# Performance work log

Measured on AMD Instinct MI355X. Metric: run time of the kernel, lower is better.

The kernel has to match this reference:

```python
import jax, jax.numpy as jnp
import numpy as np

ALPHA = (0.02, 0.04, 0.08, 0.16)
CHAMFER_W, SMOOTH_W, CURVATURE_W = 1.0, 1.0, 0.3
NS = (8192, 4096, 2048, 1024)
B = 2


def _sqdist(a, b):
    # a: [B,N,3], b: [B,M,3] -> [B,N,M] squared euclidean distance
    return (jnp.sum(a * a, axis=-1)[:, :, None]
            - 2.0 * jnp.einsum('bnc,bmc->bnm', a, b)
            + jnp.sum(b * b, axis=-1)[:, None, :])


def _knn(d, k):
    # k smallest distances + indices along last axis
    neg, idx = jax.lax.top_k(-d, k)
    return -neg, idx


def _gather(points, idx):
    # points: [B,M,C], idx: [B,N,K] -> [B,N,K,C]
    return jax.vmap(lambda p, i: p[i])(points, idx)


def _scale_loss(pc1, pc2, flow):
    # pc1, pc2, flow: [B,3,N]-like -> permute to points-last layout
    p1 = jnp.transpose(pc1, (0, 2, 1))   # [B,N,3]
    p2 = jnp.transpose(pc2, (0, 2, 1))   # [B,M,3]
    fl = jnp.transpose(flow, (0, 2, 1))  # [B,N,3]
    warp = p1 + fl                        # warped pc1

    # curvature of pc2 (10-NN on pc2 itself)
    _, k22 = _knn(_sqdist(p2, p2), 10)
    cv2 = jnp.sum(_gather(p2, k22) - p2[:, :, None, :], axis=2) / 9.0  # [B,M,3]

    # 10-NN on pc1 (shared for warped curvature and smoothness; 9-NN is prefix)
    _, k11 = _knn(_sqdist(p1, p1), 10)
    cvw = jnp.sum(_gather(warp, k11) - warp[:, :, None, :], axis=2) / 9.0  # [B,N,3]

    k9 = k11[:, :, :9]
    gfl = _gather(fl, k9)  # [B,N,9,3]
    smooth = jnp.sum(jnp.linalg.norm(gfl - fl[:, :, None, :], axis=3), axis=2) / 8.0  # [B,N]

    # chamfer between warped pc1 and pc2
    d12 = _sqdist(warp, p2)               # [B,N,M]
    dist1 = jnp.min(d12, axis=-1)         # [B,N]
    dist2 = jnp.min(d12, axis=1)          # [B,M]

    # inverse-distance interpolation of pc2 curvature onto warped pc1 (5-NN)
    dist, kidx = _knn(d12, 5)             # [B,N,5]
    gcv = _gather(cv2, kidx)              # [B,N,5,3]
    w = 1.0 / (dist + 1e-8)
    w = w / jnp.sum(w, axis=2, keepdims=True)
    inter = jnp.sum(w[..., None] * gcv, axis=2)  # [B,N,3]

    chamfer = jnp.mean(jnp.sum(dist1, axis=1)) + jnp.mean(jnp.sum(dist2, axis=1))
    smoothness = jnp.mean(jnp.sum(smooth, axis=1))
    curv = jnp.mean(jnp.sum(jnp.sum((inter - cvw) ** 2, axis=2), axis=1))
    return chamfer, smoothness, curv


def setup_inputs() -> dict:
    key = jax.random.key(0)
    keys = jax.random.split(key, 12)
    out = {}
    names = ['pc1', 'pc2', 'flow']
    k = 0
    for name in names:
        for i, n in enumerate(NS):
            scale = 1.0 if name != 'flow' else 0.1
            out[f'{name}_{i}'] = scale * jax.random.normal(keys[k], (B, 3, n), dtype=jnp.float32)
            k += 1
    return out


def reference(pc1_0, pc1_1, pc1_2, pc1_3,
              pc2_0, pc2_1, pc2_2, pc2_3,
              flow_0, flow_1, flow_2, flow_3):
    pcs1 = (pc1_0, pc1_1, pc1_2, pc1_3)
    pcs2 = (pc2_0, pc2_1, pc2_2, pc2_3)
    flows = (flow_0, flow_1, flow_2, flow_3)
    ch = sm = cv = jnp.float32(0.0)
    for a, p1, p2, fl in zip(ALPHA, pcs1, pcs2, flows):
        c, s, k = _scale_loss(p1, p2, fl)
        ch = ch + a * c
        sm = sm + a * s
        cv = cv + a * k
    total = CHAMFER_W * ch + CURVATURE_W * cv + SMOOTH_W * sm
    return jnp.reshape(total, (1,))
```

## Files before the change

### kernel.cpp

```cpp
#include <hip/hip_runtime.h>
#include <math.h>


#define BLOCK 512
#define UNIT 1024
#define NTOT 15360
#define MASKC 0xFFFFE000u
#define PB 340

typedef unsigned int uint;

struct Params {
  const float* pc1[4];
  const float* pc2[4];
  const float* fl[4];
  float4* cv2;
  float4* cvw;
  float* keys;
  float* out;
};

__device__ __forceinline__ void decode(int r, int wv, int& s, int& b,
                                       int& i0, int& lo, int& N, int& cpw,
                                       int& off, float& alpha) {
  int rr;
  if (r < 256)      { s = 0; rr = r; }
  else if (r < 320) { s = 1; rr = r - 256; }
  else if (r < 336) { s = 2; rr = r - 320; }
  else              { s = 3; rr = r - 336; }
  N = 8192 >> s;
  cpw = 8 >> s;
  int perb = 128 >> (2 * s);
  b = rr >> (7 - 2 * s);
  int chunk = rr & (perb - 1);
  int qg = (chunk << s) + (wv >> (3 - s));
  i0 = qg << 6;
  lo = (wv & (cpw - 1)) << 10;
  off = 16384 - (16384 >> s);
  alpha = 0.02f * (float)(1 << s);
}

__device__ __forceinline__ float wave_sum(float v) {
  #pragma unroll
  for (int o = 32; o; o >>= 1) v += __shfl_down(v, o, 64);
  return v;
}

template <int K>
__device__ __forceinline__ void key_insert(float (&kd)[K], float kf) {
  #pragma unroll
  for (int m = K - 1; m >= 1; --m)
    kd[m] = __builtin_amdgcn_fmed3f(kf, kd[m - 1], kd[m]);
  kd[0] = fminf(kd[0], kf);
}

template <int K>
__device__ __forceinline__ void merge_pair(float (&a)[K], const float (&b)[K]) {
  #pragma unroll
  for (int m = 0; m < K; ++m) key_insert<K>(a, b[m]);
}

__device__ __forceinline__ float pack_key(float d, float iw) {
  return __uint_as_float((__float_as_uint(d) & MASKC) | __float_as_uint(iw));
}

template <int K, bool WARP, bool PACK>
__device__ void scan_u(const float* px, const float* py, const float* pz,
                       const float* fx, const float* fy, const float* fz,
                       int lo, float ax, float ay, float az,
                       float (&a)[K], float (&b)[K], float4* tile,
                       int lane) {
  int j = lo + lane;
  float x = px[j], y = py[j], z = pz[j];
  if (WARP) { x += fx[j]; y += fy[j]; z += fz[j]; }
  for (int c0 = lo; c0 < lo + UNIT; c0 += 64) {
    tile[lane] = make_float4(x, y, z, __uint_as_float((uint)(c0 + lane)));
    asm volatile("s_waitcnt lgkmcnt(0)" ::: "memory");
    if (c0 + 64 < lo + UNIT) {
      int jn = j + 64;
      x = px[jn]; y = py[jn]; z = pz[jn];
      if (WARP) { x += fx[jn]; y += fy[jn]; z += fz[jn]; }
    }
    #pragma unroll 8
    for (int t = 0; t < 64; t += 2) {
      float4 cA = tile[t];
      float4 cB = tile[t + 1];
      float dxa = ax - cA.x, dya = ay - cA.y, dza = az - cA.z;
      float dA = fmaf(dxa, dxa, fmaf(dya, dya, dza * dza));
      float dxb = ax - cB.x, dyb = ay - cB.y, dzb = az - cB.z;
      float dB = fmaf(dxb, dxb, fmaf(dyb, dyb, dzb * dzb));
      if (PACK) {
        key_insert<K>(a, pack_key(dA, cA.w));
        key_insert<K>(b, pack_key(dB, cB.w));
      } else {
        a[0] = fminf(a[0], dA);
        b[0] = fminf(b[0], dB);
      }
    }
    j += 64;
  }
}

template <int K>
__device__ __forceinline__ bool merge_group(float (&a)[K], float* sm,
                                            int tid, int cpw) {
  const int STR = K | 1;
  int q = tid & 63, wv = tid >> 6;
  #pragma unroll
  for (int m = 0; m < K; ++m) sm[(wv * 64 + q) * STR + m] = a[m];
  __syncthreads();
  if (wv & (cpw - 1)) return false;
  for (int w = wv + 1; w < wv + cpw; ++w)
    #pragma unroll
    for (int m = 0; m < K; ++m)
      key_insert<K>(a, sm[(w * 64 + q) * STR + m]);
  return true;
}

__global__ __launch_bounds__(1) void k_zero(float* out) { out[0] = 0.f; }

__global__ __launch_bounds__(BLOCK, 8) void k_fused(Params P) {
  __shared__ float4 tiles[8][64];
  __shared__ float sm[8 * 64 * 11];
  int tid = threadIdx.x, q = tid & 63, wv = tid >> 6;
  int pass = blockIdx.x / PB, r = blockIdx.x % PB;
  int s, b, i0, lo, N, cpw, off; float alpha;
  decode(r, wv, s, b, i0, lo, N, cpw, off, alpha);
  int i = i0 + q;
  float4* tile = tiles[wv];

  if (pass == 0) {
    const float* p2 = P.pc2[s] + b * 3 * N;
    float ax = p2[i], ay = p2[N + i], az = p2[2 * N + i];
    float a[10], bb[10];
    #pragma unroll
    for (int m = 0; m < 10; ++m) { a[m] = 3.0e38f; bb[m] = 3.0e38f; }
    scan_u<10, false, true>(p2, p2 + N, p2 + 2 * N, nullptr, nullptr,
                            nullptr, lo, ax, ay, az, a, bb, tile, q);
    merge_pair<10>(a, bb);
    if (!merge_group<10>(a, sm, tid, cpw)) return;
    float sx = 0.f, sy = 0.f, sz = 0.f;
    #pragma unroll
    for (int m = 0; m < 10; ++m) {
      int j = (int)(__float_as_uint(a[m]) & 0x1FFFu);
      sx += p2[j]; sy += p2[N + j]; sz += p2[2 * N + j];
    }
    const float inv9 = 1.f / 9.f;
    P.cv2[b * NTOT + off + i] = make_float4((sx - 10.f * ax) * inv9,
                                            (sy - 10.f * ay) * inv9,
                                            (sz - 10.f * az) * inv9, 0.f);
  } else if (pass == 1) {
    const float* p1 = P.pc1[s] + b * 3 * N;
    const float* fl = P.fl[s] + b * 3 * N;
    float ax = p1[i], ay = p1[N + i], az = p1[2 * N + i];
    float a[10], bb[10];
    #pragma unroll
    for (int m = 0; m < 10; ++m) { a[m] = 3.0e38f; bb[m] = 3.0e38f; }
    scan_u<10, false, true>(p1, p1 + N, p1 + 2 * N, nullptr, nullptr,
                            nullptr, lo, ax, ay, az, a, bb, tile, q);
    merge_pair<10>(a, bb);
    if (!merge_group<10>(a, sm, tid, cpw)) return;
    float fix = fl[i], fiy = fl[N + i], fiz = fl[2 * N + i];
    float wix = ax + fix, wiy = ay + fiy, wiz = az + fiz;
    float sx = 0.f, sy = 0.f, sz = 0.f, smooth = 0.f;
    float dmax = -1.f, worst = 0.f;
    #pragma unroll
    for (int m = 0; m < 10; ++m) {
      int j = (int)(__float_as_uint(a[m]) & 0x1FFFu);
      float px = p1[j], py = p1[N + j], pz = p1[2 * N + j];
      float flx = fl[j], fly = fl[N + j], flz = fl[2 * N + j];
      sx += px + flx; sy += py + fly; sz += pz + flz;
      float ddx = px - ax, ddy = py - ay, ddz = pz - az;
      float d = fmaf(ddx, ddx, fmaf(ddy, ddy, ddz * ddz));
      float gx = flx - fix, gy = fly - fiy, gz = flz - fiz;
      float term = sqrtf(fmaf(gx, gx, fmaf(gy, gy, gz * gz)));
      smooth += term;
      if (d > dmax) { dmax = d; worst = term; }
    }
    smooth -= worst;
    const float inv9 = 1.f / 9.f;
    P.cvw[b * NTOT + off + i] = make_float4((sx - 10.f * wix) * inv9,
                                            (sy - 10.f * wiy) * inv9,
                                            (sz - 10.f * wiz) * inv9, 0.f);
    float ssum = wave_sum(smooth * (1.f / 8.f));
    if (q == 0) atomicAdd(P.out, alpha * 0.5f * ssum);
  } else if (pass == 2) {
    const float* p1 = P.pc1[s] + b * 3 * N;
    const float* fl = P.fl[s] + b * 3 * N;
    const float* p2 = P.pc2[s] + b * 3 * N;
    float ax = p2[i], ay = p2[N + i], az = p2[2 * N + i];
    float a[1], bb[1];
    a[0] = 3.0e38f; bb[0] = 3.0e38f;
    scan_u<1, true, false>(p1, p1 + N, p1 + 2 * N, fl, fl + N, fl + 2 * N,
                           lo, ax, ay, az, a, bb, tile, q);
    merge_pair<1>(a, bb);
    if (!merge_group<1>(a, sm, tid, cpw)) return;
    float msum = wave_sum(a[0]);
    if (q == 0) atomicAdd(P.out, alpha * 0.5f * msum);
  } else {
    const float* p1 = P.pc1[s] + b * 3 * N;
    const float* fl = P.fl[s] + b * 3 * N;
    const float* p2 = P.pc2[s] + b * 3 * N;
    float ax = p1[i] + fl[i], ay = p1[N + i] + fl[N + i],
          az = p1[2 * N + i] + fl[2 * N + i];
    float a[5], bb[5];
    #pragma unroll
    for (int m = 0; m < 5; ++m) { a[m] = 3.0e38f; bb[m] = 3.0e38f; }
    scan_u<5, false, true>(p2, p2 + N, p2 + 2 * N, nullptr, nullptr,
                           nullptr, lo, ax, ay, az, a, bb, tile, q);
    merge_pair<5>(a, bb);
    if (!merge_group<5>(a, sm, tid, cpw)) return;
    #pragma unroll
    for (int m = 0; m < 5; ++m)
      P.keys[m * (2 * NTOT) + b * NTOT + off + i] = a[m];
  }
}

__global__ __launch_bounds__(256) void k_epi(Params P) {
  int t = blockIdx.x * 256 + threadIdx.x;
  int b = t >= NTOT;
  int r = t - b * NTOT;
  int s, i;
  if (r < 8192)       { s = 0; i = r; }
  else if (r < 12288) { s = 1; i = r - 8192; }
  else if (r < 14336) { s = 2; i = r - 12288; }
  else                { s = 3; i = r - 14336; }
  int N = 8192 >> s;
  int off = 16384 - (16384 >> s);
  float alpha = 0.02f * (float)(1 << s);
  const float* p1 = P.pc1[s] + b * 3 * N;
  const float* fl = P.fl[s] + b * 3 * N;
  const float* p2 = P.pc2[s] + b * 3 * N;
  float ax = p1[i] + fl[i], ay = p1[N + i] + fl[N + i],
        az = p1[2 * N + i] + fl[2 * N + i];
  float dist1 = 3.0e38f, wsum = 0.f, ix = 0.f, iy = 0.f, iz = 0.f;
  #pragma unroll
  for (int m = 0; m < 5; ++m) {
    uint key = __float_as_uint(P.keys[m * (2 * NTOT) + b * NTOT + off + i]);
    int j = (int)(key & 0x1FFFu);
    float px = p2[j], py = p2[N + j], pz = p2[2 * N + j];
    float ddx = px - ax, ddy = py - ay, ddz = pz - az;
    float d = fmaf(ddx, ddx, fmaf(ddy, ddy, ddz * ddz));
    dist1 = fminf(dist1, d);
    float w = 1.f / (d + 1e-8f);
    wsum += w;
    float4 cv = P.cv2[b * NTOT + off + j];
    ix += w * cv.x; iy += w * cv.y; iz += w * cv.z;
  }
  float inv = 1.f / wsum;
  ix *= inv; iy *= inv; iz *= inv;
  float4 cw = P.cvw[b * NTOT + off + i];
  float ex = ix - cw.x, ey = iy - cw.y, ez = iz - cw.z;
  float curv = fmaf(ex, ex, fmaf(ey, ey, ez * ez));
  float v = alpha * 0.5f * (dist1 + 0.3f * curv);
  v = wave_sum(v);
  if ((threadIdx.x & 63) == 0) atomicAdd(P.out, v);
}

extern "C" void kernel_launch(void* const* d_in, const int* in_sizes, int n_in,
                              void* d_out, int out_size, void* d_ws,
                              size_t ws_size, hipStream_t stream) {
  Params P;
  for (int s = 0; s < 4; ++s) {
    P.pc1[s] = (const float*)d_in[s];
    P.pc2[s] = (const float*)d_in[4 + s];
    P.fl[s]  = (const float*)d_in[8 + s];
  }
  P.cv2 = (float4*)d_ws;
  P.cvw = (float4*)((char*)d_ws + (size_t)2 * NTOT * sizeof(float4));
  P.keys = (float*)((char*)d_ws + (size_t)4 * NTOT * sizeof(float4));
  P.out = (float*)d_out;

  k_zero<<<dim3(1), dim3(1), 0, stream>>>(P.out);
  k_fused<<<dim3(4 * PB), dim3(BLOCK), 0, stream>>>(P);
  k_epi<<<dim3((2 * NTOT) / 256), dim3(256), 0, stream>>>(P);
}
```

Measured before the change: 309.0 us.

## Stream candidate points via scalar loads instead of LDS tiles in kNN scans

The per-wave LDS tile staging of candidate points is replaced by wave-uniform scalar s_load_dwordx8 loads of eight candidates per coordinate into SGPRs, which the distance computation then uses directly. This removes LDS writes and reads and the lgkmcnt waits on the tile, and the packed index is now computed from a uniform counter instead of being stored in the tile. In exchange, every 8-candidate step waits on its scalar loads with no prefetch overlap and goes through the scalar cache, which may stall the inner loop, especially in the warped-chamfer scan that issues six loads per step.

Result: slower. 315.2 us (+2.0%).

```diff
diff --git a/kernel.cpp b/kernel.cpp
--- a/kernel.cpp
+++ b/kernel.cpp
@@ -9,6 +9,7 @@
 #define PB 340
 
 typedef unsigned int uint;
+typedef __attribute__((ext_vector_type(8))) float f8;
 
 struct Params {
   const float* pc1[4];
@@ -60,44 +61,79 @@
   for (int m = 0; m < K; ++m) key_insert<K>(a, b[m]);
 }
 
-__device__ __forceinline__ float pack_key(float d, float iw) {
-  return __uint_as_float((__float_as_uint(d) & MASKC) | __float_as_uint(iw));
-}
-
-template <int K, bool WARP, bool PACK>
-__device__ void scan_u(const float* px, const float* py, const float* pz,
+__device__ __forceinline__ float pack_key_u(float d, uint iw) {
+  return __uint_as_float((__float_as_uint(d) & MASKC) | iw);
+}
+
+__device__ __forceinline__ void sload3(const float* px, const float* py,
+                                       const float* pz, int boff,
+                                       f8& x, f8& y, f8& z) {
+  asm volatile(
+      "s_load_dwordx8 %0, %3, %6\n\t"
+      "s_load_dwordx8 %1, %4, %6\n\t"
+      "s_load_dwordx8 %2, %5, %6\n\t"
+      "s_waitcnt lgkmcnt(0)"
+      : "=&s"(x), "=&s"(y), "=&s"(z)
+      : "s"(px), "s"(py), "s"(pz), "s"(boff));
+}
+
+__device__ __forceinline__ void sload6(const float* px, const float* py,
+                                       const float* pz, const float* fx,
+                                       const float* fy, const float* fz,
+                                       int boff, f8& x, f8& y, f8& z,
+                                       f8& u, f8& v, f8& w) {
+  asm volatile(
+      "s_load_dwordx8 %0, %6, %12\n\t"
+      "s_load_dwordx8 %1, %7, %12\n\t"
+      "s_load_dwordx8 %2, %8, %12\n\t"
+      "s_load_dwordx8 %3, %9, %12\n\t"
+      "s_load_dwordx8 %4, %10, %12\n\t"
+      "s_load_dwordx8 %5, %11, %12\n\t"
+      "s_waitcnt lgkmcnt(0)"
+      : "=&s"(x), "=&s"(y), "=&s"(z), "=&s"(u), "=&s"(v), "=&s"(w)
+      : "s"(px), "s"(py), "s"(pz), "s"(fx), "s"(fy), "s"(fz), "s"(boff));
+}
+
+template <int K>
+__device__ void scan_k(const float* px, const float* py, const float* pz,
+                       int lo_u, float ax, float ay, float az,
+                       float (&a)[K], float (&b)[K]) {
+  #pragma unroll 1
+  for (int c0 = 0; c0 < UNIT; c0 += 8) {
+    f8 xs, ys, zs;
+    sload3(px, py, pz, (lo_u + c0) * 4, xs, ys, zs);
+    #pragma unroll
+    for (int t = 0; t < 8; t += 2) {
+      float dxa = xs[t] - ax, dya = ys[t] - ay, dza = zs[t] - az;
+      float dA = fmaf(dxa, dxa, fmaf(dya, dya, dza * dza));
+      float dxb = xs[t + 1] - ax, dyb = ys[t + 1] - ay, dzb = zs[t + 1] - az;
+      float dB = fmaf(dxb, dxb, fmaf(dyb, dyb, dzb * dzb));
+      key_insert<K>(a, pack_key_u(dA, (uint)(lo_u + c0 + t)));
+      key_insert<K>(b, pack_key_u(dB, (uint)(lo_u + c0 + t + 1)));
+    }
+  }
+}
+
+__device__ void scan_w(const float* px, const float* py, const float* pz,
                        const float* fx, const float* fy, const float* fz,
-                       int lo, float ax, float ay, float az,
-                       float (&a)[K], float (&b)[K], float4* tile,
-                       int lane) {
-  int j = lo + lane;
-  float x = px[j], y = py[j], z = pz[j];
-  if (WARP) { x += fx[j]; y += fy[j]; z += fz[j]; }
-  for (int c0 = lo; c0 < lo + UNIT; c0 += 64) {
-    tile[lane] = make_float4(x, y, z, __uint_as_float((uint)(c0 + lane)));
-    asm volatile("s_waitcnt lgkmcnt(0)" ::: "memory");
-    if (c0 + 64 < lo + UNIT) {
-      int jn = j + 64;
-      x = px[jn]; y = py[jn]; z = pz[jn];
-      if (WARP) { x += fx[jn]; y += fy[jn]; z += fz[jn]; }
+                       int lo_u, float ax, float ay, float az,
+                       float (&a)[1], float (&b)[1]) {
+  #pragma unroll 1
+  for (int c0 = 0; c0 < UNIT; c0 += 8) {
+    f8 xs, ys, zs, us, vs, ws;
+    sload6(px, py, pz, fx, fy, fz, (lo_u + c0) * 4, xs, ys, zs, us, vs, ws);
+    #pragma unroll
+    for (int t = 0; t < 8; t += 2) {
+      float cxa = xs[t] + us[t], cya = ys[t] + vs[t], cza = zs[t] + ws[t];
+      float dxa = cxa - ax, dya = cya - ay, dza = cza - az;
+      float dA = fmaf(dxa, dxa, fmaf(dya, dya, dza * dza));
+      float cxb = xs[t + 1] + us[t + 1], cyb = ys[t + 1] + vs[t + 1],
+            czb = zs[t + 1] + ws[t + 1];
+      float dxb = cxb - ax, dyb = cyb - ay, dzb = czb - az;
+      float dB = fmaf(dxb, dxb, fmaf(dyb, dyb, dzb * dzb));
+      a[0] = fminf(a[0], dA);
+      b[0] = fminf(b[0], dB);
     }
-    #pragma unroll 8
-    for (int t = 0; t < 64; t += 2) {
-      float4 cA = tile[t];
-      float4 cB = tile[t + 1];
-      float dxa = ax - cA.x, dya = ay - cA.y, dza = az - cA.z;
-      float dA = fmaf(dxa, dxa, fmaf(dya, dya, dza * dza));
-      float dxb = ax - cB.x, dyb = ay - cB.y, dzb = az - cB.z;
-      float dB = fmaf(dxb, dxb, fmaf(dyb, dyb, dzb * dzb));
-      if (PACK) {
-        key_insert<K>(a, pack_key(dA, cA.w));
-        key_insert<K>(b, pack_key(dB, cB.w));
-      } else {
-        a[0] = fminf(a[0], dA);
-        b[0] = fminf(b[0], dB);
-      }
-    }
-    j += 64;
   }
 }
 
@@ -120,14 +156,13 @@
 __global__ __launch_bounds__(1) void k_zero(float* out) { out[0] = 0.f; }
 
 __global__ __launch_bounds__(BLOCK, 8) void k_fused(Params P) {
-  __shared__ float4 tiles[8][64];
   __shared__ float sm[8 * 64 * 11];
   int tid = threadIdx.x, q = tid & 63, wv = tid >> 6;
   int pass = blockIdx.x / PB, r = blockIdx.x % PB;
   int s, b, i0, lo, N, cpw, off; float alpha;
   decode(r, wv, s, b, i0, lo, N, cpw, off, alpha);
   int i = i0 + q;
-  float4* tile = tiles[wv];
+  int lo_u = __builtin_amdgcn_readfirstlane(lo);
 
   if (pass == 0) {
     const float* p2 = P.pc2[s] + b * 3 * N;
@@ -135,8 +170,7 @@
     float a[10], bb[10];
     #pragma unroll
     for (int m = 0; m < 10; ++m) { a[m] = 3.0e38f; bb[m] = 3.0e38f; }
-    scan_u<10, false, true>(p2, p2 + N, p2 + 2 * N, nullptr, nullptr,
-                            nullptr, lo, ax, ay, az, a, bb, tile, q);
+    scan_k<10>(p2, p2 + N, p2 + 2 * N, lo_u, ax, ay, az, a, bb);
     merge_pair<10>(a, bb);
     if (!merge_group<10>(a, sm, tid, cpw)) return;
     float sx = 0.f, sy = 0.f, sz = 0.f;
@@ -156,8 +190,7 @@
     float a[10], bb[10];
     #pragma unroll
     for (int m = 0; m < 10; ++m) { a[m] = 3.0e38f; bb[m] = 3.0e38f; }
-    scan_u<10, false, true>(p1, p1 + N, p1 + 2 * N, nullptr, nullptr,
-                            nullptr, lo, ax, ay, az, a, bb, tile, q);
+    scan_k<10>(p1, p1 + N, p1 + 2 * N, lo_u, ax, ay, az, a, bb);
     merge_pair<10>(a, bb);
     if (!merge_group<10>(a, sm, tid, cpw)) return;
     float fix = fl[i], fiy = fl[N + i], fiz = fl[2 * N + i];
@@ -191,8 +224,8 @@
     float ax = p2[i], ay = p2[N + i], az = p2[2 * N + i];
     float a[1], bb[1];
     a[0] = 3.0e38f; bb[0] = 3.0e38f;
-    scan_u<1, true, false>(p1, p1 + N, p1 + 2 * N, fl, fl + N, fl + 2 * N,
-                           lo, ax, ay, az, a, bb, tile, q);
+    scan_w(p1, p1 + N, p1 + 2 * N, fl, fl + N, fl + 2 * N,
+           lo_u, ax, ay, az, a, bb);
     merge_pair<1>(a, bb);
     if (!merge_group<1>(a, sm, tid, cpw)) return;
     float msum = wave_sum(a[0]);
@@ -206,8 +239,7 @@
     float a[5], bb[5];
     #pragma unroll
     for (int m = 0; m < 5; ++m) { a[m] = 3.0e38f; bb[m] = 3.0e38f; }
-    scan_u<5, false, true>(p2, p2 + N, p2 + 2 * N, nullptr, nullptr,
-                           nullptr, lo, ax, ay, az, a, bb, tile, q);
+    scan_k<5>(p2, p2 + N, p2 + 2 * N, lo_u, ax, ay, az, a, bb);
     merge_pair<5>(a, bb);
     if (!merge_group<5>(a, sm, tid, cpw)) return;
     #pragma unroll
```
